# Kernel tuning notes

Hardware: AMD Instinct MI355X
Metric: run time of the kernel (lower is better)

## Reference

```python
import jax, jax.numpy as jnp
import numpy as np

B = 1024        # sessions
N = 32          # nodes per session
S = 50          # steps per session
H = 256         # hidden_size
V = 50000       # vocab size of embedding_table
GROUP = 3       # items pooled per step (reshape(-1, 3, H) in source)
SAN_BLOCKS = 3


def setup_inputs() -> dict:
    key = jax.random.key(0)
    ks = jax.random.split(key, 16)
    node_embedding = jax.random.normal(ks[0], (B * N, H), jnp.float32)
    emb_weight = jax.random.normal(ks[1], (V, H), jnp.float32) * 0.02
    batch = jnp.repeat(jnp.arange(B, dtype=jnp.int32), N)           # session id per node
    sequence = jax.random.randint(ks[2], (B * S, GROUP), 0, N + 1)  # local idx; ==N -> zero pad row
    itemset_len = jax.random.randint(ks[3], (B * S,), 1, GROUP + 1).astype(jnp.float32)
    sequence_len = jnp.full((B,), S, dtype=jnp.int32)               # steps per session
    cue = jax.random.randint(ks[4], (B,), 0, V)
    sc = 1.0 / np.sqrt(H)
    in_proj_w = jax.random.normal(ks[5], (3 * H, H), jnp.float32) * sc
    in_proj_b = jnp.zeros((3 * H,), jnp.float32)
    out_proj_w = jax.random.normal(ks[6], (H, H), jnp.float32) * sc
    out_proj_b = jnp.zeros((H,), jnp.float32)
    d1_w = jax.random.normal(ks[7], (H, H), jnp.float32) * sc
    d1_b = jnp.zeros((H,), jnp.float32)
    d2_w = jax.random.normal(ks[8], (H, H), jnp.float32) * sc
    d2_b = jnp.zeros((H,), jnp.float32)
    W3_w = jax.random.normal(ks[9], (H, 2 * H), jnp.float32) * (1.0 / np.sqrt(2 * H))
    W3_b = jnp.zeros((H,), jnp.float32)
    return {
        "node_embedding": node_embedding, "emb_weight": emb_weight,
        "itemset_len": itemset_len, "in_proj_w": in_proj_w, "in_proj_b": in_proj_b,
        "out_proj_w": out_proj_w, "out_proj_b": out_proj_b,
        "d1_w": d1_w, "d1_b": d1_b, "d2_w": d2_w, "d2_b": d2_b,
        "W3_w": W3_w, "W3_b": W3_b,
        "batch": batch, "sequence": sequence, "sequence_len": sequence_len, "cue": cue,
    }


def reference(node_embedding, emb_weight, itemset_len, in_proj_w, in_proj_b,
              out_proj_w, out_proj_b, d1_w, d1_b, d2_w, d2_b, W3_w, W3_b,
              batch, sequence, sequence_len, cue):
    # Eval mode: dropout disabled.
    total_nodes, h = node_embedding.shape
    nsess = sequence_len.shape[0]
    total_steps = sequence.shape[0]

    # Per-session node counts and exclusive offsets (replaces torch.split on ragged batch).
    sections = jnp.bincount(batch, length=nsess)
    offsets = jnp.cumsum(sections) - sections

    # Append one global zero row; local index == sections[sess] maps to it
    # (matches the per-session zero row in v_i_zeros).
    nodes_pad = jnp.concatenate([node_embedding, jnp.zeros((1, h), node_embedding.dtype)], axis=0)
    step_sess = jnp.repeat(jnp.arange(nsess), sequence_len, total_repeat_length=total_steps)
    sec_s = sections[step_sess][:, None]
    off_s = offsets[step_sess][:, None]
    gidx = jnp.where(sequence == sec_s, total_nodes, off_s + sequence)  # [T, 3] global indices

    # session_i: 3-way sum of gathered node embeddings / itemset_len  -> [T, H]
    step_emb = nodes_pad[gidx].sum(axis=1) / itemset_len[:, None]

    # Last step of each session (both v_n and the position s_g is read from).
    last_idx = jnp.cumsum(sequence_len) - 1
    v_n = step_emb[last_idx]  # [B, H]

    # nn.MultiheadAttention receives (L=1, N=steps, E=H): softmax over a single key
    # is identically 1, so MHA == out_proj(v_proj(x)) applied per step independently.
    # Hence the SAN chain on the last step equals the chain applied to v_n alone.
    Wv = in_proj_w[2 * h:]
    bv = in_proj_b[2 * h:]
    x = v_n
    for _ in range(SAN_BLOCKS):
        attn = (x @ Wv.T + bv) @ out_proj_w.T + out_proj_b
        # Residual FFN (dropout off in eval): x + d2(relu(d1(x)))
        x = attn + (jax.nn.relu(attn @ d1_w.T + d1_b) @ d2_w.T + d2_b)
    s_g = x  # [B, H]

    s_h = jnp.concatenate([v_n, s_g], axis=1) @ W3_w.T + W3_b  # [B, H]
    y_hat = jnp.sum(s_h * emb_weight[cue], axis=1)             # [B]
    all_scores = s_h @ emb_weight.T                            # [B, V]
    return y_hat, all_scores
```

## Files before the change

### kernel.cpp

```cpp
#include <hip/hip_runtime.h>
#include <hip/hip_bf16.h>
#include <stdint.h>

typedef __attribute__((ext_vector_type(8))) short short8;
typedef __attribute__((ext_vector_type(4))) short short4v;
typedef __attribute__((ext_vector_type(4))) float f32x4;

#define HD 256

__device__ __forceinline__ ushort f2bf(float f) {
  union { float f; uint32_t u; } x; x.f = f;
  uint32_t r = (x.u + 0x7fffu + ((x.u >> 16) & 1u)) >> 16;
  return (ushort)r;
}

__device__ __forceinline__ int swz(int row, int col) {
  int chunk = (col >> 3) ^ (row & 7);
  return row * 256 + chunk * 8 + (col & 7);
}

__global__ void prep1_kernel(const float* __restrict__ in_proj_w,
                             const float* __restrict__ in_proj_b,
                             const float* __restrict__ out_proj_w,
                             const float* __restrict__ out_proj_b,
                             const float* __restrict__ d1_w,
                             const float* __restrict__ d2_w,
                             const float* __restrict__ W3_w,
                             ushort* __restrict__ Wc_bf, ushort* __restrict__ d1_bf,
                             ushort* __restrict__ d2_bf, ushort* __restrict__ W3_bf,
                             float* __restrict__ bc) {
  int blk = blockIdx.x, t = threadIdx.x;
  if (blk < 256) {
    int i = blk * 256 + t;
    d1_bf[i] = f2bf(d1_w[i]);
    d2_bf[i] = f2bf(d2_w[i]);
    W3_bf[i] = f2bf(W3_w[i]);
    W3_bf[i + 65536] = f2bf(W3_w[i + 65536]);
  } else {
    int i = blk - 256;
    const float* Po = out_proj_w + i * HD;
    const float* Wv = in_proj_w + 2 * HD * HD;
    float acc = 0.f;
    for (int m = 0; m < HD; ++m) acc += Po[m] * Wv[m * HD + t];
    Wc_bf[i * HD + t] = f2bf(acc);
    if (t == 0) {
      const float* bv = in_proj_b + 2 * HD;
      float b = out_proj_b[i];
      for (int m = 0; m < HD; ++m) b += Po[m] * bv[m];
      bc[i] = b;
    }
  }
}

template<bool RELU, bool RESID, bool WACC>
__device__ __forceinline__ void gemm_stage16(const ushort* inA, const ushort* __restrict__ Wbf,
                                             const float* __restrict__ bias,
                                             float* accf, ushort* outB) {
  int t = threadIdx.x;
  int lane = t & 63, wid = t >> 6;
  int la = lane & 15, g = lane >> 4;
  int col = wid * 16 + la;
  f32x4 acc0 = {0.f, 0.f, 0.f, 0.f};
  f32x4 acc1 = {0.f, 0.f, 0.f, 0.f};
#pragma unroll
  for (int kk = 0; kk < 4; ++kk) {
    short8 a0 = *(const short8*)&inA[swz(la, kk * 32 + g * 8)];
    short8 b0 = *(const short8*)&Wbf[col * HD + kk * 32 + g * 8];
    short8 a1 = *(const short8*)&inA[swz(la, (kk + 4) * 32 + g * 8)];
    short8 b1 = *(const short8*)&Wbf[col * HD + (kk + 4) * 32 + g * 8];
    acc0 = __builtin_amdgcn_mfma_f32_16x16x32_bf16(a0, b0, acc0, 0, 0, 0);
    acc1 = __builtin_amdgcn_mfma_f32_16x16x32_bf16(a1, b1, acc1, 0, 0, 0);
  }
  float bia = bias[col];
#pragma unroll
  for (int r = 0; r < 4; ++r) {
    int ro = g * 4 + r;
    float v = acc0[r] + acc1[r] + bia;
    if (RELU) v = fmaxf(v, 0.f);
    if (RESID) v += accf[ro * HD + col];
    if (WACC) accf[ro * HD + col] = v;
    outB[swz(ro, col)] = f2bf(v);
  }
}

__device__ __forceinline__ void stage_fence() {
  __syncthreads();
  __builtin_amdgcn_sched_barrier(0);
}

__global__ __launch_bounds__(1024, 1) void sh_kernel(
    const float* __restrict__ node_emb, const float* __restrict__ emb_w,
    const float* __restrict__ itemset_len,
    const float* __restrict__ d1_b, const float* __restrict__ d2_b,
    const float* __restrict__ W3_b, const float* __restrict__ bc,
    const int* __restrict__ sequence, const int* __restrict__ cue,
    const int* __restrict__ batch, int total_nodes,
    const int* __restrict__ seq_len,
    const ushort* __restrict__ Wc_bf, const ushort* __restrict__ d1_bf,
    const ushort* __restrict__ d2_bf, const ushort* __restrict__ W3_bf,
    ushort* __restrict__ sh_bf, float* __restrict__ y_hat, int group) {
  __shared__ float accf[16 * HD];
  __shared__ ushort vn_bf[16 * HD];
  __shared__ ushort bufA[16 * HD];
  __shared__ ushort bufB[16 * HD];
  __shared__ int lbs[17];
  __shared__ int lli[16];
  int t = threadIdx.x;
  int b0 = blockIdx.x * 16;

  {
    if (t < 17) {
      int target = b0 + t;
      int lo = 0, hi = total_nodes;
      while (lo < hi) {
        int mid = (lo + hi) >> 1;
        if (batch[mid] < target) lo = mid + 1; else hi = mid;
      }
      lbs[t] = lo;
    }
    int wid = t >> 6, lane = t & 63;
    int n = b0 + wid + 1;
    int ssum = 0;
    for (int i = lane; i < n; i += 64) ssum += seq_len[i];
#pragma unroll
    for (int off = 32; off >= 1; off >>= 1) ssum += __shfl_down(ssum, off, 64);
    if (lane == 0) lli[wid] = ssum - 1;
  }
  __syncthreads();

  {
    int r = t >> 6, cg = t & 63;
    int li = lli[r];
    float inv = 1.0f / itemset_len[li];
    int off = lbs[r], sec = lbs[r + 1] - lbs[r];
    float4 s = {0.f, 0.f, 0.f, 0.f};
    for (int gi = 0; gi < group; ++gi) {
      int sq = sequence[li * group + gi];
      if (sq == sec) continue;
      float4 v = *(const float4*)(node_emb + (size_t)(off + sq) * HD + cg * 4);
      s.x += v.x; s.y += v.y; s.z += v.z; s.w += v.w;
    }
    short4v u;
    u[0] = (short)f2bf(s.x * inv); u[1] = (short)f2bf(s.y * inv);
    u[2] = (short)f2bf(s.z * inv); u[3] = (short)f2bf(s.w * inv);
    *(short4v*)&vn_bf[swz(r, cg * 4)] = u;
  }
  stage_fence();

  const ushort* x = vn_bf;
  ushort* P = bufA;
  ushort* Q = bufB;
#pragma unroll 1
  for (int sb = 0; sb < 3; ++sb) {
    gemm_stage16<false, false, true>(x, Wc_bf, bc, accf, P);
    stage_fence();
    gemm_stage16<true, false, false>(P, d1_bf, d1_b, nullptr, Q);
    stage_fence();
    gemm_stage16<false, true, false>(Q, d2_bf, d2_b, accf, P);
    stage_fence();
    x = P;
    ushort* tmp = P; P = Q; Q = tmp;
  }

  {
    int lane = t & 63, wid = t >> 6;
    int la = lane & 15, g = lane >> 4;
    int col = wid * 16 + la;
    f32x4 acc0 = {0.f, 0.f, 0.f, 0.f};
    f32x4 acc1 = {0.f, 0.f, 0.f, 0.f};
#pragma unroll
    for (int kk = 0; kk < 8; ++kk) {
      short8 a0 = *(const short8*)&vn_bf[swz(la, kk * 32 + g * 8)];
      short8 b0 = *(const short8*)&W3_bf[col * 2 * HD + kk * 32 + g * 8];
      short8 a1 = *(const short8*)&x[swz(la, kk * 32 + g * 8)];
      short8 b1 = *(const short8*)&W3_bf[col * 2 * HD + (kk + 8) * 32 + g * 8];
      acc0 = __builtin_amdgcn_mfma_f32_16x16x32_bf16(a0, b0, acc0, 0, 0, 0);
      acc1 = __builtin_amdgcn_mfma_f32_16x16x32_bf16(a1, b1, acc1, 0, 0, 0);
    }
    float bia = W3_b[col];
#pragma unroll
    for (int r = 0; r < 4; ++r) {
      int ro = g * 4 + r;
      float v = acc0[r] + acc1[r] + bia;
      accf[ro * HD + col] = v;
      sh_bf[(size_t)(b0 + ro) * HD + col] = f2bf(v);
    }
  }
  stage_fence();

  {
    int r = t >> 6, lane = t & 63;
    const float4 er = *(const float4*)(emb_w + (size_t)cue[b0 + r] * HD + lane * 4);
    const float* ar = &accf[r * HD + lane * 4];
    float p = ar[0] * er.x + ar[1] * er.y + ar[2] * er.z + ar[3] * er.w;
#pragma unroll
    for (int off = 32; off >= 1; off >>= 1) p += __shfl_down(p, off, 64);
    if (lane == 0) y_hat[b0 + r] = p;
  }
}

__global__ __launch_bounds__(256) void score_kernel(
    const ushort* __restrict__ sh_bf, const float* __restrict__ emb_w,
    float* __restrict__ scores, int nrows, int V) {
  __shared__ ushort ebuf[64 * HD];
  __shared__ float obuf[64][65];
  int t = threadIdx.x;
  int c0 = blockIdx.x * 64;
#pragma unroll
  for (int i = 0; i < 8; ++i) {
    int c = t + i * 256;
    int row = c >> 5, q = c & 31;
    if (c0 + row < V) {
      const float4* src = (const float4*)(emb_w + (size_t)(c0 + row) * HD + q * 8);
      float4 v0 = src[0], v1 = src[1];
      short8 u;
      u[0] = (short)f2bf(v0.x); u[1] = (short)f2bf(v0.y);
      u[2] = (short)f2bf(v0.z); u[3] = (short)f2bf(v0.w);
      u[4] = (short)f2bf(v1.x); u[5] = (short)f2bf(v1.y);
      u[6] = (short)f2bf(v1.z); u[7] = (short)f2bf(v1.w);
      *(short8*)&ebuf[row * 256 + ((q ^ (row & 7)) * 8)] = u;
    }
  }
  __syncthreads();

  int lane = t & 63, wid = t >> 6;
  int la = lane & 15, g = lane >> 4;
  int nrb = nrows >> 6;
  int cg = c0 + lane;
  bool cok = cg < V;

  short8 a[8];
  {
    const ushort* arow = sh_bf + (size_t)(wid * 16 + la) * HD;
#pragma unroll
    for (int kk = 0; kk < 8; ++kk) a[kk] = *(const short8*)&arow[kk * 32 + g * 8];
  }

  for (int rb = 0; rb < nrb; ++rb) {
    f32x4 acc[4] = {{0.f,0.f,0.f,0.f},{0.f,0.f,0.f,0.f},{0.f,0.f,0.f,0.f},{0.f,0.f,0.f,0.f}};
#pragma unroll
    for (int kk = 0; kk < 8; ++kk) {
#pragma unroll
      for (int ct = 0; ct < 4; ++ct) {
        int brow = ct * 16 + la;
        short8 b = *(const short8*)&ebuf[brow * 256 + (((kk * 4 + g) ^ (brow & 7)) * 8)];
        acc[ct] = __builtin_amdgcn_mfma_f32_16x16x32_bf16(a[kk], b, acc[ct], 0, 0, 0);
      }
    }
    short8 an[8];
    if (rb + 1 < nrb) {
      const ushort* arow = sh_bf + (size_t)((rb + 1) * 64 + wid * 16 + la) * HD;
#pragma unroll
      for (int kk = 0; kk < 8; ++kk) an[kk] = *(const short8*)&arow[kk * 32 + g * 8];
    }
#pragma unroll
    for (int ct = 0; ct < 4; ++ct)
#pragma unroll
      for (int r = 0; r < 4; ++r)
        obuf[wid * 16 + g * 4 + r][ct * 16 + la] = acc[ct][r];
#pragma unroll
    for (int i = 0; i < 16; ++i) {
      int row = wid * 16 + i;
      float v = obuf[row][lane];
      if (cok)
        __builtin_nontemporal_store(v, &scores[(size_t)(rb * 64 + row) * V + cg]);
    }
#pragma unroll
    for (int kk = 0; kk < 8; ++kk) a[kk] = an[kk];
  }
}

extern "C" void kernel_launch(void* const* d_in, const int* in_sizes, int n_in,
                              void* d_out, int out_size, void* d_ws, size_t ws_size,
                              hipStream_t stream) {
  const float* node_emb   = (const float*)d_in[0];
  const float* emb_w      = (const float*)d_in[1];
  const float* itemset_len= (const float*)d_in[2];
  const float* in_proj_w  = (const float*)d_in[3];
  const float* in_proj_b  = (const float*)d_in[4];
  const float* out_proj_w = (const float*)d_in[5];
  const float* out_proj_b = (const float*)d_in[6];
  const float* d1_w       = (const float*)d_in[7];
  const float* d1_b       = (const float*)d_in[8];
  const float* d2_w       = (const float*)d_in[9];
  const float* d2_b       = (const float*)d_in[10];
  const float* W3_w       = (const float*)d_in[11];
  const float* W3_b       = (const float*)d_in[12];
  const int*   batch      = (const int*)d_in[13];
  const int*   sequence   = (const int*)d_in[14];
  const int*   seq_len    = (const int*)d_in[15];
  const int*   cue        = (const int*)d_in[16];

  int total_nodes = in_sizes[0] / HD;
  int V           = in_sizes[1] / HD;
  int nsess       = in_sizes[15];
  int total_steps = in_sizes[2];
  int group       = in_sizes[14] / total_steps;

  char* ws = (char*)d_ws;
  float* bc       = (float*)(ws + 12288);
  ushort* sh_bf   = (ushort*)(ws + 16384);
  ushort* Wc_bf   = (ushort*)(ws + 16384 + 524288);
  ushort* d1_bf   = Wc_bf + HD * HD;
  ushort* d2_bf   = d1_bf + HD * HD;
  ushort* W3_bf   = d2_bf + HD * HD;

  float* y_hat  = (float*)d_out;
  float* scores = (float*)d_out + nsess;

  prep1_kernel<<<512, 256, 0, stream>>>(in_proj_w, in_proj_b, out_proj_w, out_proj_b,
                                        d1_w, d2_w, W3_w,
                                        Wc_bf, d1_bf, d2_bf, W3_bf, bc);
  sh_kernel<<<nsess / 16, 1024, 0, stream>>>(node_emb, emb_w, itemset_len,
                                             d1_b, d2_b, W3_b, bc,
                                             sequence, cue, batch, total_nodes, seq_len,
                                             Wc_bf, d1_bf, d2_bf, W3_bf,
                                             sh_bf, y_hat, group);
  score_kernel<<<(V + 63) / 64, 256, 0, stream>>>(sh_bf, emb_w, scores, nsess, V);
}
```

Measured before the change: 140.0 us.

## Retile score kernel into 2D grid keeping session rows in registers across vocab chunks

The score GEMM now runs on a 32x8 grid. Each block holds 128 session rows of s_h in registers and walks a contiguous range of 64-wide vocab chunks, instead of each block owning one vocab chunk and looping over all session rows. The goal is to stop re-reading the s_h operand from cache for every row block and to raise output tile height per block. In exchange, every embedding chunk is now loaded and converted to bf16 eight times, once per row group. Only 256 blocks of 4 waves are launched, and load, compute and store are serialised by two barriers per chunk, which may hurt latency hiding on a store-bound kernel.

Measured after the change: 212.8 us. 1.52x slower.

```diff
diff --git a/kernel.cpp b/kernel.cpp
--- a/kernel.cpp
+++ b/kernel.cpp
@@ -199,74 +199,74 @@
   }
 }
 
-__global__ __launch_bounds__(256) void score_kernel(
+__global__ __launch_bounds__(256, 2) void score_kernel(
     const ushort* __restrict__ sh_bf, const float* __restrict__ emb_w,
     float* __restrict__ scores, int nrows, int V) {
   __shared__ ushort ebuf[64 * HD];
-  __shared__ float obuf[64][65];
+  __shared__ float obuf[128][65];
   int t = threadIdx.x;
-  int c0 = blockIdx.x * 64;
-#pragma unroll
-  for (int i = 0; i < 8; ++i) {
-    int c = t + i * 256;
-    int row = c >> 5, q = c & 31;
-    if (c0 + row < V) {
-      const float4* src = (const float4*)(emb_w + (size_t)(c0 + row) * HD + q * 8);
-      float4 v0 = src[0], v1 = src[1];
-      short8 u;
-      u[0] = (short)f2bf(v0.x); u[1] = (short)f2bf(v0.y);
-      u[2] = (short)f2bf(v0.z); u[3] = (short)f2bf(v0.w);
-      u[4] = (short)f2bf(v1.x); u[5] = (short)f2bf(v1.y);
-      u[6] = (short)f2bf(v1.z); u[7] = (short)f2bf(v1.w);
-      *(short8*)&ebuf[row * 256 + ((q ^ (row & 7)) * 8)] = u;
-    }
-  }
-  __syncthreads();
-
   int lane = t & 63, wid = t >> 6;
   int la = lane & 15, g = lane >> 4;
-  int nrb = nrows >> 6;
-  int cg = c0 + lane;
-  bool cok = cg < V;
-
-  short8 a[8];
-  {
-    const ushort* arow = sh_bf + (size_t)(wid * 16 + la) * HD;
-#pragma unroll
-    for (int kk = 0; kk < 8; ++kk) a[kk] = *(const short8*)&arow[kk * 32 + g * 8];
-  }
-
-  for (int rb = 0; rb < nrb; ++rb) {
-    f32x4 acc[4] = {{0.f,0.f,0.f,0.f},{0.f,0.f,0.f,0.f},{0.f,0.f,0.f,0.f},{0.f,0.f,0.f,0.f}};
-#pragma unroll
-    for (int kk = 0; kk < 8; ++kk) {
-#pragma unroll
-      for (int ct = 0; ct < 4; ++ct) {
-        int brow = ct * 16 + la;
-        short8 b = *(const short8*)&ebuf[brow * 256 + (((kk * 4 + g) ^ (brow & 7)) * 8)];
-        acc[ct] = __builtin_amdgcn_mfma_f32_16x16x32_bf16(a[kk], b, acc[ct], 0, 0, 0);
+  int ry = blockIdx.y, cx = blockIdx.x;
+  int nchunks = (V + 63) >> 6;
+  int nch = (nchunks + gridDim.x - 1) / gridDim.x;
+  int ch0 = cx * nch;
+  int ch1 = ch0 + nch; if (ch1 > nchunks) ch1 = nchunks;
+
+  short8 a[2][8];
+#pragma unroll
+  for (int rg = 0; rg < 2; ++rg) {
+    const ushort* arow = sh_bf + (size_t)(ry * 128 + wid * 32 + rg * 16 + la) * HD;
+#pragma unroll
+    for (int kk = 0; kk < 8; ++kk) a[rg][kk] = *(const short8*)&arow[kk * 32 + g * 8];
+  }
+
+  for (int ch = ch0; ch < ch1; ++ch) {
+    int e0 = ch * 64;
+#pragma unroll
+    for (int i = 0; i < 8; ++i) {
+      int c = t + i * 256;
+      int row = c >> 5, q = c & 31;
+      if (e0 + row < V) {
+        const float4* src = (const float4*)(emb_w + (size_t)(e0 + row) * HD + q * 8);
+        float4 v0 = src[0], v1 = src[1];
+        short8 u;
+        u[0] = (short)f2bf(v0.x); u[1] = (short)f2bf(v0.y);
+        u[2] = (short)f2bf(v0.z); u[3] = (short)f2bf(v0.w);
+        u[4] = (short)f2bf(v1.x); u[5] = (short)f2bf(v1.y);
+        u[6] = (short)f2bf(v1.z); u[7] = (short)f2bf(v1.w);
+        *(short8*)&ebuf[row * 256 + ((q ^ (row & 7)) * 8)] = u;
       }
     }
-    short8 an[8];
-    if (rb + 1 < nrb) {
-      const ushort* arow = sh_bf + (size_t)((rb + 1) * 64 + wid * 16 + la) * HD;
-#pragma unroll
-      for (int kk = 0; kk < 8; ++kk) an[kk] = *(const short8*)&arow[kk * 32 + g * 8];
-    }
-#pragma unroll
-    for (int ct = 0; ct < 4; ++ct)
-#pragma unroll
-      for (int r = 0; r < 4; ++r)
-        obuf[wid * 16 + g * 4 + r][ct * 16 + la] = acc[ct][r];
-#pragma unroll
-    for (int i = 0; i < 16; ++i) {
-      int row = wid * 16 + i;
+    __syncthreads();
+#pragma unroll
+    for (int rg = 0; rg < 2; ++rg) {
+      f32x4 acc[4] = {{0.f,0.f,0.f,0.f},{0.f,0.f,0.f,0.f},{0.f,0.f,0.f,0.f},{0.f,0.f,0.f,0.f}};
+#pragma unroll
+      for (int kk = 0; kk < 8; ++kk) {
+#pragma unroll
+        for (int ct = 0; ct < 4; ++ct) {
+          int brow = ct * 16 + la;
+          short8 b = *(const short8*)&ebuf[brow * 256 + (((kk * 4 + g) ^ (brow & 7)) * 8)];
+          acc[ct] = __builtin_amdgcn_mfma_f32_16x16x32_bf16(a[rg][kk], b, acc[ct], 0, 0, 0);
+        }
+      }
+#pragma unroll
+      for (int ct = 0; ct < 4; ++ct)
+#pragma unroll
+        for (int r = 0; r < 4; ++r)
+          obuf[wid * 32 + rg * 16 + g * 4 + r][ct * 16 + la] = acc[ct][r];
+    }
+    bool cok = (e0 + lane) < V;
+#pragma unroll
+    for (int i = 0; i < 32; ++i) {
+      int row = wid * 32 + i;
       float v = obuf[row][lane];
       if (cok)
-        __builtin_nontemporal_store(v, &scores[(size_t)(rb * 64 + row) * V + cg]);
-    }
-#pragma unroll
-    for (int kk = 0; kk < 8; ++kk) a[kk] = an[kk];
+        __builtin_nontemporal_store(
+            v, &scores[(size_t)(ry * 128 + row) * V + e0 + lane]);
+    }
+    __syncthreads();
   }
 }
 
@@ -316,5 +316,6 @@
                                              sequence, cue, batch, total_nodes, seq_len,
                                              Wc_bf, d1_bf, d2_bf, W3_bf,
                                              sh_bf, y_hat, group);
-  score_kernel<<<(V + 63) / 64, 256, 0, stream>>>(sh_bf, emb_w, scores, nsess, V);
-}
+  dim3 sgrid(32, nsess / 128);
+  score_kernel<<<sgrid, 256, 0, stream>>>(sh_bf, emb_w, scores, nsess, V);
+}
```
